# Kernel optimization log

Hardware: AMD Instinct MI355X
Metric: run time of the kernel (lower is better)

Reference implementation:

```python
import jax, jax.numpy as jnp
import numpy as np
import math

D_MODEL = 1024
NHEAD = 16
HEAD_DIM = D_MODEL // NHEAD
D_FF = 4 * D_MODEL
EPS = 1e-5


def _layer_norm(x, g, b):
    mu = jnp.mean(x, axis=-1, keepdims=True)
    var = jnp.mean(jnp.square(x - mu), axis=-1, keepdims=True)
    return (x - mu) * jax.lax.rsqrt(var + EPS) * g + b


def setup_inputs() -> dict:
    key = jax.random.key(0)
    ks = jax.random.split(key, 12)
    B, N = 2, 2048
    s = 1.0 / math.sqrt(D_MODEL)
    inp = {
        "x": jax.random.normal(ks[0], (B, N, D_MODEL), dtype=jnp.float32),
        "wq": jax.random.normal(ks[1], (D_MODEL, D_MODEL), dtype=jnp.float32) * s,
        "bq": jnp.zeros((D_MODEL,), jnp.float32),
        "wk": jax.random.normal(ks[2], (D_MODEL, D_MODEL), dtype=jnp.float32) * s,
        "bk": jnp.zeros((D_MODEL,), jnp.float32),
        "wv": jax.random.normal(ks[3], (D_MODEL, D_MODEL), dtype=jnp.float32) * s,
        "bv": jnp.zeros((D_MODEL,), jnp.float32),
        "wo": jax.random.normal(ks[4], (D_MODEL, D_MODEL), dtype=jnp.float32) * s,
        "bo": jnp.zeros((D_MODEL,), jnp.float32),
        "ln1_g": jnp.ones((D_MODEL,), jnp.float32),
        "ln1_b": jnp.zeros((D_MODEL,), jnp.float32),
        "ln2_g": jnp.ones((D_MODEL,), jnp.float32),
        "ln2_b": jnp.zeros((D_MODEL,), jnp.float32),
        "w1": jax.random.normal(ks[5], (D_MODEL, D_FF), dtype=jnp.float32) * s,
        "b1": jnp.zeros((D_FF,), jnp.float32),
        "w2": jax.random.normal(ks[6], (D_FF, D_MODEL), dtype=jnp.float32) * (1.0 / math.sqrt(D_FF)),
        "b2": jnp.zeros((D_MODEL,), jnp.float32),
    }
    return inp


def reference(x, wq, bq, wk, bk, wv, bv, wo, bo, ln1_g, ln1_b, ln2_g, ln2_b, w1, b1, w2, b2):
    B, N, _ = x.shape
    normed = _layer_norm(x, ln1_g, ln1_b)
    # projections -> [B, H, N, Dh]
    q = (normed @ wq + bq).reshape(B, N, NHEAD, HEAD_DIM).transpose(0, 2, 1, 3)
    k = (normed @ wk + bk).reshape(B, N, NHEAD, HEAD_DIM).transpose(0, 2, 1, 3)
    v = (normed @ wv + bv).reshape(B, N, NHEAD, HEAD_DIM).transpose(0, 2, 1, 3)
    raw_scores = jnp.einsum("bhqd,bhkd->bhqk", q, k) / math.sqrt(HEAD_DIM)
    attn_probs = jax.nn.sigmoid(raw_scores)
    attn_out = jnp.einsum("bhqk,bhkd->bhqd", attn_probs, v) / math.sqrt(N)
    attn_out = attn_out.transpose(0, 2, 1, 3).reshape(B, N, D_MODEL)
    x = x + (attn_out @ wo + bo)  # dropout is identity in eval
    normed2 = _layer_norm(x, ln2_g, ln2_b)
    ff = jax.nn.gelu(normed2 @ w1 + b1, approximate=False) @ w2 + b2
    x = x + ff
    return (x, attn_probs)
```

## Files before the change

kernel.cpp:

```cpp
#include <hip/hip_runtime.h>
#include <hip/hip_bf16.h>
#include <math.h>

#define DMODEL 1024
#define NSEQ   2048
#define NBATCH 2
#define NHEADS 16
#define DHEAD  64
#define DFF    4096
#define MROWS  (NBATCH*NSEQ)
#define QKVLD  3072

typedef __attribute__((ext_vector_type(8))) short bf16x8;
typedef __attribute__((ext_vector_type(4))) float f32x4;

static __device__ __forceinline__ ushort f2b(float f) {
    return __builtin_bit_cast(ushort, (__bf16)f);
}

static __device__ __forceinline__ f32x4 mfma16(bf16x8 a, bf16x8 b, f32x4 c) {
    return __builtin_amdgcn_mfma_f32_16x16x32_bf16(a, b, c, 0, 0, 0);
}

static __device__ __forceinline__ void gload_lds16(const void* g, void* lds) {
    __builtin_amdgcn_global_load_lds((const __attribute__((address_space(1))) void*)g,
                                     (__attribute__((address_space(3))) void*)lds,
                                     16, 0, 0);
}

__global__ __launch_bounds__(256) void cast_tr(const float* __restrict__ W,
                                               ushort* __restrict__ Wt, int K, int Nn)
{
    const int t  = threadIdx.x;
    const int n  = blockIdx.x * 64 + (t & 63);
    const int k0 = blockIdx.y * 16 + (t >> 6) * 4;
    ushort tmp[4];
#pragma unroll
    for (int i = 0; i < 4; ++i) tmp[i] = f2b(W[(long)(k0 + i) * Nn + n]);
    *(uint2*)(Wt + (long)n * K + k0) = *(const uint2*)tmp;
}

__global__ __launch_bounds__(256) void concat3(const float* __restrict__ a,
                                               const float* __restrict__ b,
                                               const float* __restrict__ c,
                                               float* __restrict__ o)
{
    const int t = blockIdx.x * 256 + threadIdx.x;
    float v = 0.0f;
    if (t < 1024)      v = a[t];
    else if (t < 2048) v = b[t - 1024];
    else if (t < 3072) v = c[t - 2048];
    o[t] = v;
}

__global__ __launch_bounds__(256) void ln_kernel(const float* __restrict__ x,
                                                 const float* __restrict__ g,
                                                 const float* __restrict__ bb,
                                                 ushort* __restrict__ out)
{
    const int row = blockIdx.x;
    const int tid = threadIdx.x;
    const float4 v = ((const float4*)(x + (long)row * DMODEL))[tid];
    float s = v.x + v.y + v.z + v.w;
#pragma unroll
    for (int o = 32; o; o >>= 1) s += __shfl_down(s, o, 64);
    __shared__ float red[4];
    if ((tid & 63) == 0) red[tid >> 6] = s;
    __syncthreads();
    const float mu = (red[0] + red[1] + red[2] + red[3]) * (1.0f / DMODEL);
    __syncthreads();
    const float d0 = v.x - mu, d1 = v.y - mu, d2 = v.z - mu, d3 = v.w - mu;
    float s2 = d0*d0 + d1*d1 + d2*d2 + d3*d3;
#pragma unroll
    for (int o = 32; o; o >>= 1) s2 += __shfl_down(s2, o, 64);
    if ((tid & 63) == 0) red[tid >> 6] = s2;
    __syncthreads();
    const float inv = rsqrtf((red[0] + red[1] + red[2] + red[3]) * (1.0f / DMODEL) + 1e-5f);
    const float4 gg = ((const float4*)g)[tid];
    const float4 bv = ((const float4*)bb)[tid];
    ushort4 o4;
    o4.x = f2b(d0 * inv * gg.x + bv.x);
    o4.y = f2b(d1 * inv * gg.y + bv.y);
    o4.z = f2b(d2 * inv * gg.z + bv.z);
    o4.w = f2b(d3 * inv * gg.w + bv.w);
    ((ushort4*)(out + (long)row * DMODEL))[tid] = o4;
}

template<bool GELU>
__global__ __launch_bounds__(512, 2) void gemm8(const ushort* __restrict__ A, int lda,
                                                const ushort* __restrict__ Bt, int ldb,
                                                const float* __restrict__ bias,
                                                ushort* __restrict__ C, int ldc, int K)
{
    extern __shared__ char smem[];
    const int tid  = threadIdx.x;
    const int lane = tid & 63;
    const int w    = tid >> 6;
    const int wm   = w >> 2;
    const int wn   = w & 3;
    const long row0 = (long)blockIdx.x * 256;
    const long col0 = (long)blockIdx.y * 256;

    const int srow = tid >> 2;
    const int scol = (tid & 3) * 8;
    const ushort* Ag = A  + (row0 + srow) * (long)lda + scol;
    const ushort* Bg = Bt + (col0 + srow) * (long)ldb + scol;

#define STAGE_A8(buf, k0)                                                                  \
    do {                                                                                   \
        gload_lds16(Ag + (k0),                  smem + ((buf) << 14) + w * 1024);          \
        gload_lds16(Ag + 128 * (long)lda + (k0), smem + ((buf) << 14) + 8192 + w * 1024);  \
    } while (0)
#define STAGE_B8(buf, k0)                                                                  \
    do {                                                                                   \
        gload_lds16(Bg + (k0),                  smem + 65536 + ((buf) << 14) + w * 1024);  \
        gload_lds16(Bg + 128 * (long)ldb + (k0), smem + 65536 + ((buf) << 14) + 8192 + w * 1024); \
    } while (0)

    const f32x4 zero = {0.f, 0.f, 0.f, 0.f};
    f32x4 acc[8][4];
#pragma unroll
    for (int m = 0; m < 8; ++m)
#pragma unroll
        for (int j = 0; j < 4; ++j) acc[m][j] = zero;

    const int NT = K >> 5;
    STAGE_A8(0, 0);  STAGE_B8(0, 0);
    STAGE_A8(1, 32); STAGE_B8(1, 32);

    const int abase = (wm * 128 + (lane & 15)) * 32 + (lane >> 4) * 8;
    const int bbase = (wn * 64  + (lane & 15)) * 32 + (lane >> 4) * 8;

    for (int t = 0; t < NT; ++t) {
        if (t == NT - 1) asm volatile("s_waitcnt vmcnt(0)" ::: "memory");
        else             asm volatile("s_waitcnt vmcnt(4)" ::: "memory");
        __builtin_amdgcn_sched_barrier(0);
        __builtin_amdgcn_s_barrier();
        __builtin_amdgcn_sched_barrier(0);

        const ushort* Abase = (const ushort*)(smem + ((t & 3) << 14));
        const ushort* Bbase = (const ushort*)(smem + 65536 + ((t & 3) << 14));

        bf16x8 bfr[4], afr[4];
#pragma unroll
        for (int ni = 0; ni < 4; ++ni)
            bfr[ni] = *(const bf16x8*)&Bbase[bbase + ni * 512];
#pragma unroll
        for (int mi = 0; mi < 4; ++mi)
            afr[mi] = *(const bf16x8*)&Abase[abase + mi * 512];
        if (t + 2 < NT) STAGE_A8((t + 2) & 3, (t + 2) * 32);
        __builtin_amdgcn_s_setprio(1);
#pragma unroll
        for (int mi = 0; mi < 4; ++mi)
#pragma unroll
            for (int ni = 0; ni < 4; ++ni)
                acc[mi][ni] = mfma16(afr[mi], bfr[ni], acc[mi][ni]);
        __builtin_amdgcn_s_setprio(0);

#pragma unroll
        for (int mi = 0; mi < 4; ++mi)
            afr[mi] = *(const bf16x8*)&Abase[abase + (mi + 4) * 512];
        if (t + 2 < NT) STAGE_B8((t + 2) & 3, (t + 2) * 32);
        __builtin_amdgcn_s_setprio(1);
#pragma unroll
        for (int mi = 0; mi < 4; ++mi)
#pragma unroll
            for (int ni = 0; ni < 4; ++ni)
                acc[mi + 4][ni] = mfma16(afr[mi], bfr[ni], acc[mi + 4][ni]);
        __builtin_amdgcn_s_setprio(0);
    }
#undef STAGE_A8
#undef STAGE_B8

#pragma unroll
    for (int ni = 0; ni < 4; ++ni) {
        const int colg = (int)col0 + wn * 64 + ni * 16 + (lane & 15);
        const float bcol = bias[colg];
#pragma unroll
        for (int mi = 0; mi < 8; ++mi) {
#pragma unroll
            for (int r = 0; r < 4; ++r) {
                const long rowg = row0 + wm * 128 + mi * 16 + (lane >> 4) * 4 + r;
                float vv = acc[mi][ni][r] + bcol;
                if (GELU) vv = 0.5f * vv * (1.0f + erff(vv * 0.70710678118f));
                C[rowg * ldc + colg] = f2b(vv);
            }
        }
    }
}

template<bool OUTF32, bool GELU, bool RES>
__global__ __launch_bounds__(256, 2) void gemm4p(const ushort* __restrict__ A, int lda,
                                                 const ushort* __restrict__ Bt, int ldb,
                                                 const float* __restrict__ bias,
                                                 const float* __restrict__ res,
                                                 void* __restrict__ Cout,
                                                 int Nn, int K)
{
    extern __shared__ char smem[];
    const int tid  = threadIdx.x;
    const int lane = tid & 63;
    const int w    = tid >> 6;
    const int wm   = w >> 1, wn = w & 1;
    const long row0 = (long)blockIdx.x * 128;
    const long col0 = (long)blockIdx.y * 128;
    const int mrow = lane & 15;
    const int kof  = (lane >> 4) * 8;

    const int srow = tid >> 2;
    const int soff = (tid & 3) * 8;
    const ushort* Ag = A  + (row0 + srow) * (long)lda + soff;
    const ushort* Bg = Bt + (col0 + srow) * (long)ldb + soff;

#define STAGE4(buf, k0)                                                                     \
    do {                                                                                    \
        gload_lds16(Ag + (k0),                  smem + ((buf) << 13) + w * 1024);           \
        gload_lds16(Ag + 64 * (long)lda + (k0), smem + ((buf) << 13) + 4096 + w * 1024);    \
        gload_lds16(Bg + (k0),                  smem + 32768 + ((buf) << 13) + w * 1024);   \
        gload_lds16(Bg + 64 * (long)ldb + (k0), smem + 32768 + ((buf) << 13) + 4096 + w * 1024); \
    } while (0)

    const f32x4 zero = {0.f, 0.f, 0.f, 0.f};
    f32x4 acc[4][4];
#pragma unroll
    for (int m = 0; m < 4; ++m)
#pragma unroll
        for (int j = 0; j < 4; ++j) acc[m][j] = zero;

    const int NT = K >> 5;
    STAGE4(0, 0);
    STAGE4(1, 32);
    STAGE4(2, 64);

    const int abase = (wm * 64 + mrow) * 32 + kof;
    const int bbase = (wn * 64 + mrow) * 32 + kof;

    for (int t = 0; t < NT; ++t) {
        if      (t >= NT - 1) asm volatile("s_waitcnt vmcnt(0)" ::: "memory");
        else if (t == NT - 2) asm volatile("s_waitcnt vmcnt(4)" ::: "memory");
        else                  asm volatile("s_waitcnt vmcnt(8)" ::: "memory");
        __builtin_amdgcn_sched_barrier(0);
        __builtin_amdgcn_s_barrier();
        __builtin_amdgcn_sched_barrier(0);

        if (t + 3 < NT) STAGE4((t + 3) & 3, (t + 3) * 32);

        const ushort* Abase = (const ushort*)(smem + ((t & 3) << 13));
        const ushort* Bbase = (const ushort*)(smem + 32768 + ((t & 3) << 13));
        bf16x8 af[4], bfv[4];
#pragma unroll
        for (int m = 0; m < 4; ++m)
            af[m] = *(const bf16x8*)&Abase[abase + m * 512];
#pragma unroll
        for (int j = 0; j < 4; ++j)
            bfv[j] = *(const bf16x8*)&Bbase[bbase + j * 512];
        __builtin_amdgcn_s_setprio(1);
#pragma unroll
        for (int m = 0; m < 4; ++m)
#pragma unroll
            for (int j = 0; j < 4; ++j)
                acc[m][j] = mfma16(af[m], bfv[j], acc[m][j]);
        __builtin_amdgcn_s_setprio(0);
    }
#undef STAGE4

#pragma unroll
    for (int j = 0; j < 4; ++j) {
        const int colg  = (int)col0 + wn * 64 + j * 16 + mrow;
        const float bcol = bias[colg];
#pragma unroll
        for (int m = 0; m < 4; ++m) {
#pragma unroll
            for (int r = 0; r < 4; ++r) {
                const long rowg = row0 + wm * 64 + m * 16 + (lane >> 4) * 4 + r;
                float vv = acc[m][j][r] + bcol;
                if (RES)   vv += res[rowg * Nn + colg];
                if (GELU)  vv = 0.5f * vv * (1.0f + erff(vv * 0.70710678118f));
                if (OUTF32) ((float*)Cout)[rowg * Nn + colg] = vv;
                else        ((ushort*)Cout)[rowg * Nn + colg] = f2b(vv);
            }
        }
    }
}

__global__ __launch_bounds__(256) void transpose_v(const ushort* __restrict__ v,
                                                   ushort* __restrict__ vt)
{
    __shared__ ushort t[64][72];
    const int nb = blockIdx.x, bh = blockIdx.y, b = bh >> 4;
    const int hcol = (bh & 15) * DHEAD;
    const int tid  = threadIdx.x;
    const int rrow = tid >> 3;
    const int cch  = (tid & 7) * 8;
#pragma unroll
    for (int r = 0; r < 2; ++r) {
        const int nr = rrow + r * 32;
        *(uint4*)&t[nr][cch] =
            *(const uint4*)(v + ((long)(b * NSEQ + nb * 64 + nr)) * QKVLD + hcol + cch);
    }
    __syncthreads();
#pragma unroll
    for (int r = 0; r < 2; ++r) {
        const int d = rrow + r * 32;
        ushort tmp[8];
#pragma unroll
        for (int i = 0; i < 8; ++i) tmp[i] = t[cch + i][d];
        *(uint4*)(vt + ((long)bh * DHEAD + d) * NSEQ + nb * 64 + cch) = *(const uint4*)tmp;
    }
}

__global__ __launch_bounds__(256) void attn_kernel(const ushort* __restrict__ qkv,
                                                   const ushort* __restrict__ vt,
                                                   float* __restrict__ probs,
                                                   ushort* __restrict__ ao)
{
    __shared__ ushort Ks[64][72];
    __shared__ ushort Vs[64][72];
    __shared__ __align__(16) float Pf[4][16][68];
    const int tid  = threadIdx.x;
    const int lane = tid & 63;
    const int w    = tid >> 6;
    const int qb   = blockIdx.x;
    const int bh   = blockIdx.y;
    const int b    = bh >> 4;
    const int q0   = qb * 64 + w * 16;
    const int mrow = lane & 15;
    const int kof  = (lane >> 4) * 8;
    const int hcol = (bh & 15) * DHEAD;
    const int NT   = NSEQ / 64;

    bf16x8 aq0, aq1;
    {
        const ushort* qp = qkv + ((long)(b * NSEQ + q0 + mrow)) * QKVLD + hcol;
        aq0 = *(const bf16x8*)(qp + kof);
        aq1 = *(const bf16x8*)(qp + 32 + kof);
    }

    const f32x4 zero = {0.f, 0.f, 0.f, 0.f};
    f32x4 acco[4];
#pragma unroll
    for (int dj = 0; dj < 4; ++dj) acco[dj] = zero;

    const int srow = tid >> 3;
    const int sch  = (tid & 7) * 8;
    const ushort* km = qkv + 1024;

    uint4 kr0, kr1, vr0, vr1;
#define LOADT(kt)                                                                          \
    do {                                                                                   \
        kr0 = *(const uint4*)(km + ((long)(b * NSEQ + (kt) * 64 + srow)) * QKVLD + hcol + sch);       \
        kr1 = *(const uint4*)(km + ((long)(b * NSEQ + (kt) * 64 + srow + 32)) * QKVLD + hcol + sch);  \
        vr0 = *(const uint4*)(vt + ((long)bh * DHEAD + srow) * NSEQ + (kt) * 64 + sch);               \
        vr1 = *(const uint4*)(vt + ((long)bh * DHEAD + srow + 32) * NSEQ + (kt) * 64 + sch);          \
    } while (0)

    LOADT(0);

    for (int kt = 0; kt < NT; ++kt) {
        *(uint4*)&Ks[srow][sch]      = kr0;
        *(uint4*)&Ks[srow + 32][sch] = kr1;
        *(uint4*)&Vs[srow][sch]      = vr0;
        *(uint4*)&Vs[srow + 32][sch] = vr1;
        __syncthreads();
        if (kt + 1 < NT) LOADT(kt + 1);

        f32x4 s[4];
#pragma unroll
        for (int j = 0; j < 4; ++j) s[j] = zero;
#pragma unroll
        for (int j = 0; j < 4; ++j) {
            bf16x8 b0 = *(const bf16x8*)&Ks[j * 16 + mrow][kof];
            bf16x8 b1 = *(const bf16x8*)&Ks[j * 16 + mrow][32 + kof];
            s[j] = mfma16(aq0, b0, s[j]);
            s[j] = mfma16(aq1, b1, s[j]);
        }

#pragma unroll
        for (int j = 0; j < 4; ++j) {
#pragma unroll
            for (int r = 0; r < 4; ++r) {
                const int rr = (lane >> 4) * 4 + r;
                const float e  = __expf(-0.125f * s[j][r]);
                const float pv = __builtin_amdgcn_rcpf(1.0f + e);
                Pf[w][rr][j * 16 + mrow] = pv;
            }
        }

        const long pbase = ((long)(bh * NSEQ + q0)) * NSEQ + kt * 64;
#pragma unroll
        for (int i = 0; i < 4; ++i) {
            const int rr = (lane >> 4) + 4 * i;
            const float4 pv4 = *(const float4*)&Pf[w][rr][mrow * 4];
            *(float4*)(probs + pbase + (long)rr * NSEQ + mrow * 4) = pv4;
        }

#pragma unroll
        for (int ks = 0; ks < 2; ++ks) {
            const float4 f0 = *(const float4*)&Pf[w][mrow][ks * 32 + kof];
            const float4 f1 = *(const float4*)&Pf[w][mrow][ks * 32 + kof + 4];
            bf16x8 ap;
            ap[0] = (short)f2b(f0.x); ap[1] = (short)f2b(f0.y);
            ap[2] = (short)f2b(f0.z); ap[3] = (short)f2b(f0.w);
            ap[4] = (short)f2b(f1.x); ap[5] = (short)f2b(f1.y);
            ap[6] = (short)f2b(f1.z); ap[7] = (short)f2b(f1.w);
#pragma unroll
            for (int dj = 0; dj < 4; ++dj) {
                bf16x8 bv = *(const bf16x8*)&Vs[dj * 16 + mrow][ks * 32 + kof];
                acco[dj] = mfma16(ap, bv, acco[dj]);
            }
        }
        __syncthreads();
    }
#undef LOADT

    const float sc = rsqrtf((float)NSEQ);
#pragma unroll
    for (int dj = 0; dj < 4; ++dj)
#pragma unroll
        for (int r = 0; r < 4; ++r) {
            const int rr = (lane >> 4) * 4 + r;
            ao[((long)(b * NSEQ + q0 + rr)) * DMODEL + hcol + dj * 16 + mrow] =
                f2b(acco[dj][r] * sc);
        }
}

extern "C" void kernel_launch(void* const* d_in, const int* in_sizes, int n_in,
                              void* d_out, int out_size, void* d_ws, size_t ws_size,
                              hipStream_t stream) {
    (void)in_sizes; (void)n_in; (void)out_size;
    const float* x    = (const float*)d_in[0];
    const float* wq   = (const float*)d_in[1];
    const float* bq   = (const float*)d_in[2];
    const float* wk   = (const float*)d_in[3];
    const float* bk   = (const float*)d_in[4];
    const float* wv   = (const float*)d_in[5];
    const float* bv   = (const float*)d_in[6];
    const float* wo   = (const float*)d_in[7];
    const float* bo   = (const float*)d_in[8];
    const float* ln1g = (const float*)d_in[9];
    const float* ln1b = (const float*)d_in[10];
    const float* ln2g = (const float*)d_in[11];
    const float* ln2b = (const float*)d_in[12];
    const float* w1   = (const float*)d_in[13];
    const float* b1   = (const float*)d_in[14];
    const float* w2   = (const float*)d_in[15];
    const float* b2   = (const float*)d_in[16];

    char* ws = (char*)d_ws;
    const size_t MB = 1u << 20;
    ushort* wqkv_t  = (ushort*)(ws + 0 * MB);
    ushort* wo_t    = (ushort*)(ws + 6 * MB);
    ushort* w1_t    = (ushort*)(ws + 8 * MB);
    ushort* w2_t    = (ushort*)(ws + 16 * MB);
    float*  bqkv    = (float*) (ws + 24 * MB);
    ushort* normed  = (ushort*)(ws + 25 * MB);
    ushort* qkvbuf  = (ushort*)(ws + 33 * MB);
    ushort* vtb     = (ushort*)(ws + 57 * MB);
    ushort* attn_o  = (ushort*)(ws + 65 * MB);
    float*  x1      = (float*) (ws + 41 * MB);
    ushort* normed2 = (ushort*)(ws + 25 * MB);
    ushort* hbuf    = (ushort*)(ws + 57 * MB);
    const float* bzero = bqkv + 3072;
    const bool fullff = (ws_size >= 90 * MB);

    float* xout  = (float*)d_out;
    float* probs = xout + (size_t)MROWS * DMODEL;

    cast_tr<<<dim3(16, 64), 256, 0, stream>>>(wq, wqkv_t,                DMODEL, DMODEL);
    cast_tr<<<dim3(16, 64), 256, 0, stream>>>(wk, wqkv_t + 1024 * 1024,  DMODEL, DMODEL);
    cast_tr<<<dim3(16, 64), 256, 0, stream>>>(wv, wqkv_t + 2048 * 1024,  DMODEL, DMODEL);
    cast_tr<<<dim3(16, 64), 256, 0, stream>>>(wo, wo_t,                  DMODEL, DMODEL);
    cast_tr<<<dim3(64, 64), 256, 0, stream>>>(w1, w1_t, DMODEL, DFF);
    cast_tr<<<dim3(16, 256), 256, 0, stream>>>(w2, w2_t, DFF, DMODEL);
    concat3<<<16, 256, 0, stream>>>(bq, bk, bv, bqkv);

    ln_kernel<<<MROWS, 256, 0, stream>>>(x, ln1g, ln1b, normed);

    gemm8<false><<<dim3(16, 12), 512, 128 * 1024, stream>>>(
        normed, DMODEL, wqkv_t, DMODEL, bqkv, qkvbuf, QKVLD, DMODEL);

    transpose_v<<<dim3(NSEQ / 64, NBATCH * NHEADS), 256, 0, stream>>>(qkvbuf + 2048, vtb);

    attn_kernel<<<dim3(NSEQ / 64, NBATCH * NHEADS), 256, 0, stream>>>(
        qkvbuf, vtb, probs, attn_o);

    gemm4p<true, false, true><<<dim3(32, 8), 256, 64 * 1024, stream>>>(
        attn_o, DMODEL, wo_t, DMODEL, bo, x, x1, DMODEL, DMODEL);

    ln_kernel<<<MROWS, 256, 0, stream>>>(x1, ln2g, ln2b, normed2);

    if (fullff) {
        gemm8<true><<<dim3(16, 16), 512, 128 * 1024, stream>>>(
            normed2, DMODEL, w1_t, DMODEL, b1, hbuf, DFF, DMODEL);
        gemm4p<true, false, true><<<dim3(32, 8), 256, 64 * 1024, stream>>>(
            hbuf, DFF, w2_t, DFF, b2, x1, xout, DMODEL, DFF);
    } else {
        gemm8<true><<<dim3(16, 8), 512, 128 * 1024, stream>>>(
            normed2, DMODEL, w1_t, DMODEL, b1, hbuf, 2048, DMODEL);
        gemm4p<true, false, true><<<dim3(32, 8), 256, 64 * 1024, stream>>>(
            hbuf, 2048, w2_t, DFF, b2, x1, xout, DMODEL, 2048);
        gemm8<true><<<dim3(16, 8), 512, 128 * 1024, stream>>>(
            normed2, DMODEL, w1_t + 2048 * 1024, DMODEL, b1 + 2048, hbuf, 2048, DMODEL);
        gemm4p<true, false, true><<<dim3(32, 8), 256, 64 * 1024, stream>>>(
            hbuf, 2048, w2_t + 2048, DFF, bzero, xout, xout, DMODEL, 2048);
    }
}
```

Baseline: 386.7 us.

## Split-K across two warp groups in output GEMMs and fuse prep kernels

The 128x128 output-projection and FFN2 GEMMs now use 512-thread blocks where two 256-thread groups each process half of K into separate LDS buffers. The partial sums are reduced through shared memory before the bias, residual and store epilogue. This adds in-block parallelism for the 256-block grids, at the cost of double the LDS, an exchange step, and idle threads in the epilogue. Separately, the six weight cast/transpose launches, the bias concat and the first LayerNorm are merged into one prep kernel to cut launch overhead.

```diff
diff --git a/kernel.cpp b/kernel.cpp
--- a/kernel.cpp
+++ b/kernel.cpp
@@ -28,29 +28,91 @@
                                      16, 0, 0);
 }
 
-__global__ __launch_bounds__(256) void cast_tr(const float* __restrict__ W,
-                                               ushort* __restrict__ Wt, int K, int Nn)
-{
-    const int t  = threadIdx.x;
-    const int n  = blockIdx.x * 64 + (t & 63);
-    const int k0 = blockIdx.y * 16 + (t >> 6) * 4;
+static __device__ __forceinline__ void cast_tile(const float* __restrict__ W,
+                                                 ushort* __restrict__ Wt,
+                                                 int K, int Nn, int bx, int by, int t)
+{
+    const int n  = bx * 64 + (t & 63);
+    const int k0 = by * 16 + (t >> 6) * 4;
     ushort tmp[4];
 #pragma unroll
     for (int i = 0; i < 4; ++i) tmp[i] = f2b(W[(long)(k0 + i) * Nn + n]);
     *(uint2*)(Wt + (long)n * K + k0) = *(const uint2*)tmp;
 }
 
-__global__ __launch_bounds__(256) void concat3(const float* __restrict__ a,
-                                               const float* __restrict__ b,
-                                               const float* __restrict__ c,
-                                               float* __restrict__ o)
-{
-    const int t = blockIdx.x * 256 + threadIdx.x;
-    float v = 0.0f;
-    if (t < 1024)      v = a[t];
-    else if (t < 2048) v = b[t - 1024];
-    else if (t < 3072) v = c[t - 2048];
-    o[t] = v;
+__global__ __launch_bounds__(256) void prep(const float* __restrict__ wq,
+                                            const float* __restrict__ wk,
+                                            const float* __restrict__ wv,
+                                            const float* __restrict__ wo,
+                                            const float* __restrict__ w1,
+                                            const float* __restrict__ w2,
+                                            const float* __restrict__ bq,
+                                            const float* __restrict__ bk,
+                                            const float* __restrict__ bv,
+                                            const float* __restrict__ x,
+                                            const float* __restrict__ ln1g,
+                                            const float* __restrict__ ln1b,
+                                            ushort* __restrict__ wqkv_t,
+                                            ushort* __restrict__ wo_t,
+                                            ushort* __restrict__ w1_t,
+                                            ushort* __restrict__ w2_t,
+                                            float* __restrict__ bqkv,
+                                            ushort* __restrict__ normed)
+{
+    __shared__ float red[4];
+    const int id  = blockIdx.x;
+    const int tid = threadIdx.x;
+
+    if (id < 1024) {
+        cast_tile(wq, wqkv_t, 1024, 1024, id & 15, id >> 4, tid);
+    } else if (id < 2048) {
+        const int i2 = id - 1024;
+        cast_tile(wk, wqkv_t + 1024 * 1024, 1024, 1024, i2 & 15, i2 >> 4, tid);
+    } else if (id < 3072) {
+        const int i2 = id - 2048;
+        cast_tile(wv, wqkv_t + 2048 * 1024, 1024, 1024, i2 & 15, i2 >> 4, tid);
+    } else if (id < 4096) {
+        const int i2 = id - 3072;
+        cast_tile(wo, wo_t, 1024, 1024, i2 & 15, i2 >> 4, tid);
+    } else if (id < 8192) {
+        const int i2 = id - 4096;
+        cast_tile(w1, w1_t, 1024, 4096, i2 & 63, i2 >> 6, tid);
+    } else if (id < 12288) {
+        const int i2 = id - 8192;
+        cast_tile(w2, w2_t, 4096, 1024, i2 & 15, i2 >> 4, tid);
+    } else if (id < 12304) {
+        const int t = (id - 12288) * 256 + tid;
+        float v = 0.0f;
+        if (t < 1024)      v = bq[t];
+        else if (t < 2048) v = bk[t - 1024];
+        else if (t < 3072) v = bv[t - 2048];
+        bqkv[t] = v;
+    } else {
+        const int row = id - 12304;
+        const float4 v = ((const float4*)(x + (long)row * DMODEL))[tid];
+        float s = v.x + v.y + v.z + v.w;
+#pragma unroll
+        for (int o = 32; o; o >>= 1) s += __shfl_down(s, o, 64);
+        if ((tid & 63) == 0) red[tid >> 6] = s;
+        __syncthreads();
+        const float mu = (red[0] + red[1] + red[2] + red[3]) * (1.0f / DMODEL);
+        __syncthreads();
+        const float d0 = v.x - mu, d1 = v.y - mu, d2 = v.z - mu, d3 = v.w - mu;
+        float s2 = d0*d0 + d1*d1 + d2*d2 + d3*d3;
+#pragma unroll
+        for (int o = 32; o; o >>= 1) s2 += __shfl_down(s2, o, 64);
+        if ((tid & 63) == 0) red[tid >> 6] = s2;
+        __syncthreads();
+        const float inv = rsqrtf((red[0] + red[1] + red[2] + red[3]) * (1.0f / DMODEL) + 1e-5f);
+        const float4 gg = ((const float4*)ln1g)[tid];
+        const float4 bv4 = ((const float4*)ln1b)[tid];
+        ushort4 o4;
+        o4.x = f2b(d0 * inv * gg.x + bv4.x);
+        o4.y = f2b(d1 * inv * gg.y + bv4.y);
+        o4.z = f2b(d2 * inv * gg.z + bv4.z);
+        o4.w = f2b(d3 * inv * gg.w + bv4.w);
+        ((ushort4*)(normed + (long)row * DMODEL))[tid] = o4;
+    }
 }
 
 __global__ __launch_bounds__(256) void ln_kernel(const float* __restrict__ x,
@@ -190,7 +252,7 @@
 }
 
 template<bool OUTF32, bool GELU, bool RES>
-__global__ __launch_bounds__(256, 2) void gemm4p(const ushort* __restrict__ A, int lda,
+__global__ __launch_bounds__(512, 2) void gemm4s(const ushort* __restrict__ A, int lda,
                                                  const ushort* __restrict__ Bt, int ldb,
                                                  const float* __restrict__ bias,
                                                  const float* __restrict__ res,
@@ -200,24 +262,29 @@
     extern __shared__ char smem[];
     const int tid  = threadIdx.x;
     const int lane = tid & 63;
-    const int w    = tid >> 6;
-    const int wm   = w >> 1, wn = w & 1;
+    const int g    = tid >> 8;
+    const int tg   = tid & 255;
+    const int w4   = tg >> 6;
+    const int wm   = w4 >> 1, wn = w4 & 1;
     const long row0 = (long)blockIdx.x * 128;
     const long col0 = (long)blockIdx.y * 128;
     const int mrow = lane & 15;
     const int kof  = (lane >> 4) * 8;
 
-    const int srow = tid >> 2;
-    const int soff = (tid & 3) * 8;
-    const ushort* Ag = A  + (row0 + srow) * (long)lda + soff;
-    const ushort* Bg = Bt + (col0 + srow) * (long)ldb + soff;
-
-#define STAGE4(buf, k0)                                                                     \
-    do {                                                                                    \
-        gload_lds16(Ag + (k0),                  smem + ((buf) << 13) + w * 1024);           \
-        gload_lds16(Ag + 64 * (long)lda + (k0), smem + ((buf) << 13) + 4096 + w * 1024);    \
-        gload_lds16(Bg + (k0),                  smem + 32768 + ((buf) << 13) + w * 1024);   \
-        gload_lds16(Bg + 64 * (long)ldb + (k0), smem + 32768 + ((buf) << 13) + 4096 + w * 1024); \
+    const int srow = tg >> 2;
+    const int soff = (tg & 3) * 8;
+    const int kb   = g * (K >> 1);
+    const ushort* Ag = A  + (row0 + srow) * (long)lda + kb + soff;
+    const ushort* Bg = Bt + (col0 + srow) * (long)ldb + kb + soff;
+    char* Als = smem + g * 32768;
+    char* Bls = smem + 65536 + g * 32768;
+
+#define STAGE4S(buf, k0)                                                          \
+    do {                                                                          \
+        gload_lds16(Ag + (k0),                  Als + ((buf) << 13) + w4 * 1024); \
+        gload_lds16(Ag + 64 * (long)lda + (k0), Als + ((buf) << 13) + 4096 + w4 * 1024); \
+        gload_lds16(Bg + (k0),                  Bls + ((buf) << 13) + w4 * 1024); \
+        gload_lds16(Bg + 64 * (long)ldb + (k0), Bls + ((buf) << 13) + 4096 + w4 * 1024); \
     } while (0)
 
     const f32x4 zero = {0.f, 0.f, 0.f, 0.f};
@@ -227,26 +294,26 @@
 #pragma unroll
         for (int j = 0; j < 4; ++j) acc[m][j] = zero;
 
-    const int NT = K >> 5;
-    STAGE4(0, 0);
-    STAGE4(1, 32);
-    STAGE4(2, 64);
+    const int NT2 = K >> 6;
+    STAGE4S(0, 0);
+    STAGE4S(1, 32);
+    STAGE4S(2, 64);
 
     const int abase = (wm * 64 + mrow) * 32 + kof;
     const int bbase = (wn * 64 + mrow) * 32 + kof;
 
-    for (int t = 0; t < NT; ++t) {
-        if      (t >= NT - 1) asm volatile("s_waitcnt vmcnt(0)" ::: "memory");
-        else if (t == NT - 2) asm volatile("s_waitcnt vmcnt(4)" ::: "memory");
-        else                  asm volatile("s_waitcnt vmcnt(8)" ::: "memory");
+    for (int t = 0; t < NT2; ++t) {
+        if      (t >= NT2 - 1) asm volatile("s_waitcnt vmcnt(0)" ::: "memory");
+        else if (t == NT2 - 2) asm volatile("s_waitcnt vmcnt(4)" ::: "memory");
+        else                   asm volatile("s_waitcnt vmcnt(8)" ::: "memory");
         __builtin_amdgcn_sched_barrier(0);
         __builtin_amdgcn_s_barrier();
         __builtin_amdgcn_sched_barrier(0);
 
-        if (t + 3 < NT) STAGE4((t + 3) & 3, (t + 3) * 32);
-
-        const ushort* Abase = (const ushort*)(smem + ((t & 3) << 13));
-        const ushort* Bbase = (const ushort*)(smem + 32768 + ((t & 3) << 13));
+        if (t + 3 < NT2) STAGE4S((t + 3) & 3, (t + 3) * 32);
+
+        const ushort* Abase = (const ushort*)(Als + ((t & 3) << 13));
+        const ushort* Bbase = (const ushort*)(Bls + ((t & 3) << 13));
         bf16x8 af[4], bfv[4];
 #pragma unroll
         for (int m = 0; m < 4; ++m)
@@ -262,22 +329,36 @@
                 acc[m][j] = mfma16(af[m], bfv[j], acc[m][j]);
         __builtin_amdgcn_s_setprio(0);
     }
-#undef STAGE4
-
-#pragma unroll
-    for (int j = 0; j < 4; ++j) {
-        const int colg  = (int)col0 + wn * 64 + j * 16 + mrow;
-        const float bcol = bias[colg];
-#pragma unroll
-        for (int m = 0; m < 4; ++m) {
-#pragma unroll
-            for (int r = 0; r < 4; ++r) {
-                const long rowg = row0 + wm * 64 + m * 16 + (lane >> 4) * 4 + r;
-                float vv = acc[m][j][r] + bcol;
-                if (RES)   vv += res[rowg * Nn + colg];
-                if (GELU)  vv = 0.5f * vv * (1.0f + erff(vv * 0.70710678118f));
-                if (OUTF32) ((float*)Cout)[rowg * Nn + colg] = vv;
-                else        ((ushort*)Cout)[rowg * Nn + colg] = f2b(vv);
+#undef STAGE4S
+
+    __syncthreads();
+    float* xch = (float*)smem;
+    if (g == 1) {
+#pragma unroll
+        for (int m = 0; m < 4; ++m)
+#pragma unroll
+            for (int j = 0; j < 4; ++j)
+#pragma unroll
+                for (int r = 0; r < 4; ++r)
+                    xch[(m * 16 + j * 4 + r) * 256 + tg] = acc[m][j][r];
+    }
+    __syncthreads();
+    if (g == 0) {
+#pragma unroll
+        for (int j = 0; j < 4; ++j) {
+            const int colg  = (int)col0 + wn * 64 + j * 16 + mrow;
+            const float bcol = bias[colg];
+#pragma unroll
+            for (int m = 0; m < 4; ++m) {
+#pragma unroll
+                for (int r = 0; r < 4; ++r) {
+                    const long rowg = row0 + wm * 64 + m * 16 + (lane >> 4) * 4 + r;
+                    float vv = acc[m][j][r] + xch[(m * 16 + j * 4 + r) * 256 + tg] + bcol;
+                    if (RES)   vv += res[rowg * Nn + colg];
+                    if (GELU)  vv = 0.5f * vv * (1.0f + erff(vv * 0.70710678118f));
+                    if (OUTF32) ((float*)Cout)[rowg * Nn + colg] = vv;
+                    else        ((ushort*)Cout)[rowg * Nn + colg] = f2b(vv);
+                }
             }
         }
     }
@@ -466,15 +547,9 @@
     float* xout  = (float*)d_out;
     float* probs = xout + (size_t)MROWS * DMODEL;
 
-    cast_tr<<<dim3(16, 64), 256, 0, stream>>>(wq, wqkv_t,                DMODEL, DMODEL);
-    cast_tr<<<dim3(16, 64), 256, 0, stream>>>(wk, wqkv_t + 1024 * 1024,  DMODEL, DMODEL);
-    cast_tr<<<dim3(16, 64), 256, 0, stream>>>(wv, wqkv_t + 2048 * 1024,  DMODEL, DMODEL);
-    cast_tr<<<dim3(16, 64), 256, 0, stream>>>(wo, wo_t,                  DMODEL, DMODEL);
-    cast_tr<<<dim3(64, 64), 256, 0, stream>>>(w1, w1_t, DMODEL, DFF);
-    cast_tr<<<dim3(16, 256), 256, 0, stream>>>(w2, w2_t, DFF, DMODEL);
-    concat3<<<16, 256, 0, stream>>>(bq, bk, bv, bqkv);
-
-    ln_kernel<<<MROWS, 256, 0, stream>>>(x, ln1g, ln1b, normed);
+    prep<<<16400, 256, 0, stream>>>(wq, wk, wv, wo, w1, w2, bq, bk, bv,
+                                    x, ln1g, ln1b,
+                                    wqkv_t, wo_t, w1_t, w2_t, bqkv, normed);
 
     gemm8<false><<<dim3(16, 12), 512, 128 * 1024, stream>>>(
         normed, DMODEL, wqkv_t, DMODEL, bqkv, qkvbuf, QKVLD, DMODEL);
@@ -484,7 +559,7 @@
     attn_kernel<<<dim3(NSEQ / 64, NBATCH * NHEADS), 256, 0, stream>>>(
         qkvbuf, vtb, probs, attn_o);
 
-    gemm4p<true, false, true><<<dim3(32, 8), 256, 64 * 1024, stream>>>(
+    gemm4s<true, false, true><<<dim3(32, 8), 512, 128 * 1024, stream>>>(
         attn_o, DMODEL, wo_t, DMODEL, bo, x, x1, DMODEL, DMODEL);
 
     ln_kernel<<<MROWS, 256, 0, stream>>>(x1, ln2g, ln2b, normed2);
@@ -492,16 +567,16 @@
     if (fullff) {
         gemm8<true><<<dim3(16, 16), 512, 128 * 1024, stream>>>(
             normed2, DMODEL, w1_t, DMODEL, b1, hbuf, DFF, DMODEL);
-        gemm4p<true, false, true><<<dim3(32, 8), 256, 64 * 1024, stream>>>(
+        gemm4s<true, false, true><<<dim3(32, 8), 512, 128 * 1024, stream>>>(
             hbuf, DFF, w2_t, DFF, b2, x1, xout, DMODEL, DFF);
     } else {
         gemm8<true><<<dim3(16, 8), 512, 128 * 1024, stream>>>(
             normed2, DMODEL, w1_t, DMODEL, b1, hbuf, 2048, DMODEL);
-        gemm4p<true, false, true><<<dim3(32, 8), 256, 64 * 1024, stream>>>(
+        gemm4s<true, false, true><<<dim3(32, 8), 512, 128 * 1024, stream>>>(
             hbuf, 2048, w2_t, DFF, b2, x1, xout, DMODEL, 2048);
         gemm8<true><<<dim3(16, 8), 512, 128 * 1024, stream>>>(
             normed2, DMODEL, w1_t + 2048 * 1024, DMODEL, b1 + 2048, hbuf, 2048, DMODEL);
-        gemm4p<true, false, true><<<dim3(32, 8), 256, 64 * 1024, stream>>>(
+        gemm4s<true, false, true><<<dim3(32, 8), 512, 128 * 1024, stream>>>(
             hbuf, 2048, w2_t + 2048, DFF, bzero, xout, xout, DMODEL, 2048);
     }
 }
```

Result: no change. 380.2 us (-1.7%).
